# Performance work log

Hardware: AMD Instinct MI355X
Metric: run time of the kernel (lower is better)

Reference implementation:

```python
import jax, jax.numpy as jnp
import numpy as np
from jax import lax

ITER_ = 3
SMOOTH = 1e-05

B, C, D, H, W = 2, 3, 128, 160, 160


def _maxpool_axis(x, axis):
    # 3-wide max pool along one axis, stride 1, pad 1 (torch pads with -inf for max pool)
    win = [1] * x.ndim
    win[axis] = 3
    pad = [(0, 0)] * x.ndim
    pad[axis] = (1, 1)
    return lax.reduce_window(x, -jnp.inf, lax.max, tuple(win), (1,) * x.ndim, tuple(pad))


def _soft_erode(x):
    # min over axis-aligned erosions (erode = -maxpool(-x))
    nx = -x
    p1 = -_maxpool_axis(nx, 2)
    p2 = -_maxpool_axis(nx, 3)
    p3 = -_maxpool_axis(nx, 4)
    return jnp.minimum(jnp.minimum(p1, p2), p3)


def _soft_dilate(x):
    pad = ((0, 0), (0, 0), (1, 1), (1, 1), (1, 1))
    return lax.reduce_window(x, -jnp.inf, lax.max, (1, 1, 3, 3, 3), (1,) * 5, pad)


def _soft_open(x):
    return _soft_dilate(_soft_erode(x))


def _soft_skel(x):
    skel = jax.nn.relu(x - _soft_open(x))
    x_work = x
    for _ in range(ITER_):
        x_work = _soft_erode(x_work)
        delta = jax.nn.relu(x_work - _soft_open(x_work))
        skel = skel + jax.nn.relu(delta - skel * delta)
    return skel


def setup_inputs() -> dict:
    key = jax.random.key(0)
    k1, k2 = jax.random.split(key)
    net_output = jax.random.uniform(k1, (B, C, D, H, W), dtype=jnp.float32)
    target = jax.random.randint(k2, (B, 1, D, H, W), 0, C, dtype=jnp.int64)
    return {"net_output": net_output, "target": target}


def reference(net_output, target):
    num_classes = net_output.shape[1]
    labels = jnp.clip(target[:, 0], 0, num_classes - 1)
    target_1h = jax.nn.one_hot(labels, num_classes, dtype=net_output.dtype)  # [B,D,H,W,C]
    target_1h = jnp.moveaxis(target_1h, -1, 1)  # [B,C,D,H,W]

    # include_background=False, num_classes > 1 -> drop background channel
    pred = net_output[:, 1:]
    gt = target_1h[:, 1:]

    skel_pred = _soft_skel(pred)
    skel_gt = _soft_skel(gt)

    dims = (2, 3, 4)
    tprec = (jnp.sum(skel_pred * gt, dims) + SMOOTH) / (jnp.sum(skel_pred, dims) + SMOOTH)
    tsens = (jnp.sum(skel_gt * pred, dims) + SMOOTH) / (jnp.sum(skel_gt, dims) + SMOOTH)
    cl_dice = (2.0 * tprec * tsens + SMOOTH) / (tprec + tsens + SMOOTH)
    return 1.0 - jnp.mean(cl_dice)
```

## Files before the change

### kernel.cpp

```cpp
#include <hip/hip_runtime.h>
#include <math.h>

#define D_ 128
#define H_ 160
#define W_ 160
#define HW_ (H_ * W_)
#define V_ (D_ * H_ * W_)
#define SMOOTHF 1e-5

#define R_ 16
#define TY 10
#define ZC 16
#define COLS 40
#define NT 640
#define LROW 41
#define NYT 16
#define NZC 8
#define NTB (NYT * NZC)

__device__ __forceinline__ float max3f(float a, float b, float c) { return fmaxf(fmaxf(a, b), c); }
__device__ __forceinline__ float min3f(float a, float b, float c) { return fminf(fminf(a, b), c); }
__device__ __forceinline__ float4 f4min(float4 a, float4 b) {
    return make_float4(fminf(a.x,b.x), fminf(a.y,b.y), fminf(a.z,b.z), fminf(a.w,b.w));
}
__device__ __forceinline__ float4 f4max(float4 a, float4 b) {
    return make_float4(fmaxf(a.x,b.x), fmaxf(a.y,b.y), fmaxf(a.z,b.z), fmaxf(a.w,b.w));
}
__device__ __forceinline__ float4 min3x(float l, float4 c, float r) {
    return make_float4(min3f(l,c.x,c.y), min3f(c.x,c.y,c.z), min3f(c.y,c.z,c.w), min3f(c.z,c.w,r));
}
__device__ __forceinline__ float4 max3x(float l, float4 c, float r) {
    return make_float4(max3f(l,c.x,c.y), max3f(c.x,c.y,c.z), max3f(c.y,c.z,c.w), max3f(c.z,c.w,r));
}
__device__ __forceinline__ float4 relu4sub(float4 a, float4 b) {
    return make_float4(fmaxf(a.x-b.x,0.f), fmaxf(a.y-b.y,0.f), fmaxf(a.z-b.z,0.f), fmaxf(a.w-b.w,0.f));
}
__device__ __forceinline__ float4 skel_upd(float4 s, float4 d) {
    return make_float4(s.x + fmaxf(d.x - s.x*d.x, 0.f), s.y + fmaxf(d.y - s.y*d.y, 0.f),
                       s.z + fmaxf(d.z - s.z*d.z, 0.f), s.w + fmaxf(d.w - s.w*d.w, 0.f));
}

__device__ __forceinline__ float4 load_src4(const float* __restrict__ net,
                                            const int* __restrict__ tgt,
                                            int i, long p) {
    if (i < 4) {
        int b = i >> 1, c = (i & 1) + 1;
        return *(const float4*)(net + (long)(b * 3 + c) * V_ + p);
    } else {
        int j = i - 4;
        int b = j >> 1, c = (j & 1) + 1;
        int4 t = *(const int4*)(tgt + (long)b * V_ + p);
        float4 o;
        int tx = t.x < 0 ? 0 : (t.x > 2 ? 2 : t.x);
        int ty = t.y < 0 ? 0 : (t.y > 2 ? 2 : t.y);
        int tz = t.z < 0 ? 0 : (t.z > 2 ? 2 : t.z);
        int tw = t.w < 0 ? 0 : (t.w > 2 ? 2 : t.w);
        o.x = (tx == c) ? 1.0f : 0.0f;
        o.y = (ty == c) ? 1.0f : 0.0f;
        o.z = (tz == c) ? 1.0f : 0.0f;
        o.w = (tw == c) ? 1.0f : 0.0f;
        return o;
    }
}

template <int VAR>
__global__ __launch_bounds__(NT, 4) void fused_pair(
    const float* __restrict__ net, const int* __restrict__ tgt, int i0,
    const float* __restrict__ e_in, float* __restrict__ e_out,
    float* __restrict__ skel, float* __restrict__ partials) {

    __shared__ float4 Pb[2][R_ * LROW];
    __shared__ float4 E1b[2][R_ * LROW];
    __shared__ float4 E2b[R_ * LROW];
    __shared__ float smr[NT / 64][2];

    const int j = blockIdx.y, i = i0 + j;
    const int bx = blockIdx.x;
    const int y0 = (bx % NYT) * TY;
    const int z0 = (bx / NYT) * ZC;
    const int tid = threadIdx.x;
    const int r  = tid / COLS;
    const int x4 = tid - r * COLS;
    const int y  = y0 - 3 + r;
    const bool yok  = (y >= 0 && y < H_);
    const bool ymok = (y - 1 >= 0 && y - 1 < H_);
    const bool ypok = (y + 1 >= 0 && y + 1 < H_);
    const int rm = (r > 0) ? r - 1 : 0;
    const int rp = (r < R_ - 1) ? r + 1 : R_ - 1;
    const int xm = (x4 > 0) ? x4 - 1 : 0;
    const int xp = (x4 < COLS - 1) ? x4 + 1 : COLS - 1;
    const bool fxm = (x4 > 0), fxp = (x4 < COLS - 1);
    const bool rout = (r >= 3 && r < 3 + TY);
    const long colbase = (long)(yok ? y : 0) * W_ + x4 * 4;

    const float* ein_v = (VAR == 1) ? e_in + (long)j * V_ : nullptr;
    float* eout_v = (VAR == 0) ? e_out + (long)j * V_ : nullptr;
    float* skel_v = skel + (long)j * V_;
    const int ipart = (i < 4) ? (i + 4) : (i - 4);

    const float4 INF4  = make_float4( INFINITY,  INFINITY,  INFINITY,  INFINITY);
    const float4 NINF4 = make_float4(-INFINITY, -INFINITY, -INFINITY, -INFINITY);

    float4 a0 = INF4, a1 = INF4, a2 = INF4;
    float4 e11 = NINF4, e12 = NINF4;
    float4 x1a = NINF4, x1b = NINF4;
    float4 x2a = NINF4, x2b = NINF4;
    float4 psk = make_float4(0,0,0,0), ppr = make_float4(0,0,0,0);
    float acc0 = 0.f, acc1 = 0.f;

    for (int s = z0 - 3; s <= z0 + ZC + 2; ++s) {
        float4 anew;
        {
            const bool zok = (s >= 0 && s < D_);
            float4 v = INF4;
            if (zok && yok) {
                long p = (long)s * HW_ + colbase;
                v = (VAR == 0) ? load_src4(net, tgt, i, p)
                               : *(const float4*)(ein_v + p);
            }
            Pb[s & 1][r * LROW + x4] = v;
            anew = v;
            if (VAR == 1) {
                int z3 = s - 3;
                if (z3 >= z0 && z3 < z0 + ZC && rout) {
                    long p = (long)z3 * HW_ + colbase;
                    psk = *(const float4*)(skel_v + p);
                    ppr = load_src4(net, tgt, ipart, p);
                }
            }
        }

        float4 fe1;
        {
            const int z1 = s - 1;
            const bool z1ok = (z1 >= 0 && z1 < D_);
            const float4* Pp = Pb[z1 & 1];
            float4 up = Pp[rm * LROW + x4];
            float4 dn = Pp[rp * LROW + x4];
            float lf = Pp[r * LROW + xm].w;
            float rt = Pp[r * LROW + xp].x;
            if (!ymok) up = INF4;
            if (!ypok) dn = INF4;
            if (!fxm) lf = INFINITY;
            if (!fxp) rt = INFINITY;
            float4 e = f4min(f4min(min3x(lf, a2, rt), f4min(up, dn)), f4min(a1, anew));
            if (!z1ok || !yok) e = NINF4;
            fe1 = e;
            E1b[z1 & 1][r * LROW + x4] = e;
        }
        __syncthreads();

        float4 fe2, f1;
        {
            const int z2 = s - 2;
            const bool z2ok = (z2 >= 0 && z2 < D_);
            const float4* Ep = E1b[z2 & 1];
            float4 n00 = Ep[rm*LROW+xm], n01 = Ep[rm*LROW+x4], n02 = Ep[rm*LROW+xp];
            float4 n10 = Ep[r *LROW+xm],                        n12 = Ep[r *LROW+xp];
            float4 n20 = Ep[rp*LROW+xm], n21 = Ep[rp*LROW+x4], n22 = Ep[rp*LROW+xp];
            float4 c = e12;
            {
                float4 up = ymok ? n01 : INF4;
                float4 dn = ypok ? n21 : INF4;
                float lf = fxm ? n10.w : INFINITY;
                float rt = fxp ? n12.x : INFINITY;
                float4 zu = (z2 >= 1)     ? e11 : INF4;
                float4 zd = (z2 + 1 < D_) ? fe1 : INF4;
                float4 e = f4min(f4min(min3x(lf, c, rt), f4min(up, dn)), f4min(zu, zd));
                if (!z2ok || !yok) e = NINF4;
                fe2 = e;
            }
            {
                float l0 = fxm ? n00.w : -INFINITY, r0 = fxp ? n02.x : -INFINITY;
                float l1 = fxm ? n10.w : -INFINITY, r1 = fxp ? n12.x : -INFINITY;
                float l2 = fxm ? n20.w : -INFINITY, r2 = fxp ? n22.x : -INFINITY;
                float4 m = f4max(f4max(max3x(l0, n01, r0), max3x(l1, c, r1)), max3x(l2, n21, r2));
                if (!z2ok) m = NINF4;
                f1 = m;
            }
            E2b[r * LROW + x4] = fe2;
            if (VAR == 0 && z2 >= z0 && z2 < z0 + ZC && rout) {
                *(float4*)(eout_v + (long)z2 * HW_ + colbase) = fe2;
            }
        }
        __syncthreads();

        float4 f2;
        {
            float4 m00 = E2b[rm*LROW+xm], m01 = E2b[rm*LROW+x4], m02 = E2b[rm*LROW+xp];
            float4 m10 = E2b[r *LROW+xm],                         m12 = E2b[r *LROW+xp];
            float4 m20 = E2b[rp*LROW+xm], m21 = E2b[rp*LROW+x4], m22 = E2b[rp*LROW+xp];
            float l0 = fxm ? m00.w : -INFINITY, r0 = fxp ? m02.x : -INFINITY;
            float l1 = fxm ? m10.w : -INFINITY, r1 = fxp ? m12.x : -INFINITY;
            float l2 = fxm ? m20.w : -INFINITY, r2 = fxp ? m22.x : -INFINITY;
            f2 = f4max(f4max(max3x(l0, m01, r0), max3x(l1, fe2, r1)), max3x(l2, m21, r2));
        }
        {
            const int z3 = s - 3;
            if (z3 >= z0 && z3 < z0 + ZC && rout) {
                float4 dil1 = f4max(f4max(x1a, x1b), f1);
                float4 dil2 = f4max(f4max(x2a, x2b), f2);
                float4 cin = a0, ce1 = e11;
                long p = (long)z3 * HW_ + colbase;
                if (VAR == 0) {
                    float4 s0 = relu4sub(cin, dil1);
                    float4 d1 = relu4sub(ce1, dil2);
                    *(float4*)(skel_v + p) = skel_upd(s0, d1);
                } else {
                    float4 d2 = relu4sub(cin, dil1);
                    float4 sp = skel_upd(psk, d2);
                    float4 d3 = relu4sub(ce1, dil2);
                    float4 fin = skel_upd(sp, d3);
                    acc0 += fin.x * ppr.x + fin.y * ppr.y + fin.z * ppr.z + fin.w * ppr.w;
                    acc1 += fin.x + fin.y + fin.z + fin.w;
                }
            }
        }
        a0 = a1; a1 = a2; a2 = anew;
        e11 = e12; e12 = fe1;
        x1a = x1b; x1b = f1;
        x2a = x2b; x2b = f2;
    }

    if (VAR == 1) {
        #pragma unroll
        for (int off = 32; off > 0; off >>= 1) {
            acc0 += __shfl_down(acc0, off);
            acc1 += __shfl_down(acc1, off);
        }
        int wid = tid >> 6, lane = tid & 63;
        __syncthreads();
        if (lane == 0) { smr[wid][0] = acc0; smr[wid][1] = acc1; }
        __syncthreads();
        if (tid == 0) {
            float t0 = 0.f, t1 = 0.f;
            #pragma unroll
            for (int w = 0; w < NT / 64; ++w) { t0 += smr[w][0]; t1 += smr[w][1]; }
            long base = ((long)i * NTB + bx) * 2;
            partials[base + 0] = t0;
            partials[base + 1] = t1;
        }
    }
}

__global__ void reduce_partials_kernel(const float* __restrict__ partials,
                                       int i0,
                                       double* __restrict__ sums) {
    int i = i0 + blockIdx.x;
    int t = threadIdx.x;
    long base = ((long)i * NTB + t) * 2;
    double v0 = (double)partials[base + 0];
    double v1 = (double)partials[base + 1];
    #pragma unroll
    for (int off = 32; off > 0; off >>= 1) {
        v0 += __shfl_down(v0, off);
        v1 += __shfl_down(v1, off);
    }
    __shared__ double sm[2][2];
    int wid = t >> 6, lane = t & 63;
    if (lane == 0) { sm[wid][0] = v0; sm[wid][1] = v1; }
    __syncthreads();
    if (t == 0) {
        sums[2 * i + 0] = sm[0][0] + sm[1][0];
        sums[2 * i + 1] = sm[0][1] + sm[1][1];
    }
}

__global__ void finalize_kernel(const double* __restrict__ sums,
                                float* __restrict__ out) {
    if (threadIdx.x == 0 && blockIdx.x == 0) {
        double acc = 0.0;
        #pragma unroll
        for (int i = 0; i < 4; ++i) {
            double tprec = (sums[2 * i + 0] + SMOOTHF) / (sums[2 * i + 1] + SMOOTHF);
            double tsens = (sums[2 * (i + 4) + 0] + SMOOTHF) / (sums[2 * (i + 4) + 1] + SMOOTHF);
            double cl = (2.0 * tprec * tsens + SMOOTHF) / (tprec + tsens + SMOOTHF);
            acc += cl;
        }
        out[0] = (float)(1.0 - acc * 0.25);
    }
}

extern "C" void kernel_launch(void* const* d_in, const int* in_sizes, int n_in,
                              void* d_out, int out_size, void* d_ws, size_t ws_size,
                              hipStream_t stream) {
    const float* net = (const float*)d_in[0];
    const int* tgt = (const int*)d_in[1];
    float* out = (float*)d_out;

    char* ws = (char*)d_ws;
    double* sums = (double*)ws;
    float* partials = (float*)(ws + 256);
    size_t head = 256 + (size_t)8 * NTB * 2 * sizeof(float);
    head = (head + 255) & ~(size_t)255;
    float* base = (float*)(ws + head);

    size_t perVol = (size_t)2 * V_ * sizeof(float);
    int G = 1;
    if (ws_size >= head + perVol * 8) G = 8;
    else if (ws_size >= head + perVol * 4) G = 4;
    else if (ws_size >= head + perVol * 2) G = 2;

    dim3 blk(NT);
    dim3 grd(NTB, G);

    for (int i0 = 0; i0 < 8; i0 += G) {
        float* SKEL = base;
        float* E2buf = base + (size_t)G * V_;

        fused_pair<0><<<grd, blk, 0, stream>>>(net, tgt, i0, nullptr, E2buf, SKEL, nullptr);
        fused_pair<1><<<grd, blk, 0, stream>>>(net, tgt, i0, E2buf, nullptr, SKEL, partials);

        reduce_partials_kernel<<<G, 128, 0, stream>>>(partials, i0, sums);
    }

    finalize_kernel<<<1, 64, 0, stream>>>(sums, out);
}
```

Baseline: 342.3 us.

## Skew stencil pipeline stages to use one barrier per slab

Double-buffers the second erosion buffer and staggers the erode/dilate stages by one z-step so only a single __syncthreads per slab iteration is needed instead of two. The center input value and the skeleton/partner loads are now fetched from global memory at output time rather than carried in registers. This is meant to cut barrier stalls and register pressure. In exchange it adds an extra loop iteration, more shared memory, and redundant global reads.

```diff
diff --git a/kernel.cpp b/kernel.cpp
--- a/kernel.cpp
+++ b/kernel.cpp
@@ -71,7 +71,7 @@
 
     __shared__ float4 Pb[2][R_ * LROW];
     __shared__ float4 E1b[2][R_ * LROW];
-    __shared__ float4 E2b[R_ * LROW];
+    __shared__ float4 E2b[2][R_ * LROW];
     __shared__ float smr[NT / 64][2];
 
     const int j = blockIdx.y, i = i0 + j;
@@ -101,37 +101,27 @@
     const float4 INF4  = make_float4( INFINITY,  INFINITY,  INFINITY,  INFINITY);
     const float4 NINF4 = make_float4(-INFINITY, -INFINITY, -INFINITY, -INFINITY);
 
-    float4 a0 = INF4, a1 = INF4, a2 = INF4;
-    float4 e11 = NINF4, e12 = NINF4;
-    float4 x1a = NINF4, x1b = NINF4;
+    float4 p1 = INF4, p2 = INF4;
+    float4 b1 = NINF4, b2 = NINF4, b3 = NINF4;
+    float4 c1 = NINF4;
+    float4 x1a = NINF4, x1b = NINF4, x1c = NINF4;
     float4 x2a = NINF4, x2b = NINF4;
-    float4 psk = make_float4(0,0,0,0), ppr = make_float4(0,0,0,0);
     float acc0 = 0.f, acc1 = 0.f;
 
-    for (int s = z0 - 3; s <= z0 + ZC + 2; ++s) {
-        float4 anew;
-        {
+    for (int s = z0 - 3; s <= z0 + ZC + 3; ++s) {
+        float4 anew = INF4;
+        if (s <= z0 + ZC + 2) {
             const bool zok = (s >= 0 && s < D_);
-            float4 v = INF4;
             if (zok && yok) {
                 long p = (long)s * HW_ + colbase;
-                v = (VAR == 0) ? load_src4(net, tgt, i, p)
-                               : *(const float4*)(ein_v + p);
-            }
-            Pb[s & 1][r * LROW + x4] = v;
-            anew = v;
-            if (VAR == 1) {
-                int z3 = s - 3;
-                if (z3 >= z0 && z3 < z0 + ZC && rout) {
-                    long p = (long)z3 * HW_ + colbase;
-                    psk = *(const float4*)(skel_v + p);
-                    ppr = load_src4(net, tgt, ipart, p);
-                }
-            }
-        }
-
-        float4 fe1;
-        {
+                anew = (VAR == 0) ? load_src4(net, tgt, i, p)
+                                  : *(const float4*)(ein_v + p);
+            }
+            Pb[s & 1][r * LROW + x4] = anew;
+        }
+
+        float4 fe1 = NINF4;
+        if (s >= z0 - 1 && s <= z0 + ZC + 2) {
             const int z1 = s - 1;
             const bool z1ok = (z1 >= 0 && z1 < D_);
             const float4* Pp = Pb[z1 & 1];
@@ -143,70 +133,79 @@
             if (!ypok) dn = INF4;
             if (!fxm) lf = INFINITY;
             if (!fxp) rt = INFINITY;
-            float4 e = f4min(f4min(min3x(lf, a2, rt), f4min(up, dn)), f4min(a1, anew));
+            float4 e = f4min(f4min(min3x(lf, p1, rt), f4min(up, dn)), f4min(p2, anew));
             if (!z1ok || !yok) e = NINF4;
             fe1 = e;
             E1b[z1 & 1][r * LROW + x4] = e;
         }
-        __syncthreads();
-
-        float4 fe2, f1;
-        {
+
+        float4 fe2 = NINF4, f1 = NINF4;
+        if (s >= z0 + 1 && s <= z0 + ZC + 2) {
             const int z2 = s - 2;
             const bool z2ok = (z2 >= 0 && z2 < D_);
             const float4* Ep = E1b[z2 & 1];
-            float4 n00 = Ep[rm*LROW+xm], n01 = Ep[rm*LROW+x4], n02 = Ep[rm*LROW+xp];
-            float4 n10 = Ep[r *LROW+xm],                        n12 = Ep[r *LROW+xp];
-            float4 n20 = Ep[rp*LROW+xm], n21 = Ep[rp*LROW+x4], n22 = Ep[rp*LROW+xp];
-            float4 c = e12;
+            float4 n01 = Ep[rm * LROW + x4];
+            float4 n21 = Ep[rp * LROW + x4];
+            float4 c = b1;
+            float l0 = fxm ? Ep[rm * LROW + xm].w : -INFINITY;
+            float r0 = fxp ? Ep[rm * LROW + xp].x : -INFINITY;
+            float l1 = fxm ? Ep[r  * LROW + xm].w : -INFINITY;
+            float r1 = fxp ? Ep[r  * LROW + xp].x : -INFINITY;
+            float l2 = fxm ? Ep[rp * LROW + xm].w : -INFINITY;
+            float r2 = fxp ? Ep[rp * LROW + xp].x : -INFINITY;
             {
                 float4 up = ymok ? n01 : INF4;
                 float4 dn = ypok ? n21 : INF4;
-                float lf = fxm ? n10.w : INFINITY;
-                float rt = fxp ? n12.x : INFINITY;
-                float4 zu = (z2 >= 1)     ? e11 : INF4;
+                float lf = fxm ? l1 : INFINITY;
+                float rt = fxp ? r1 : INFINITY;
+                float4 zu = (z2 >= 1)     ? b2  : INF4;
                 float4 zd = (z2 + 1 < D_) ? fe1 : INF4;
                 float4 e = f4min(f4min(min3x(lf, c, rt), f4min(up, dn)), f4min(zu, zd));
                 if (!z2ok || !yok) e = NINF4;
                 fe2 = e;
             }
             {
-                float l0 = fxm ? n00.w : -INFINITY, r0 = fxp ? n02.x : -INFINITY;
-                float l1 = fxm ? n10.w : -INFINITY, r1 = fxp ? n12.x : -INFINITY;
-                float l2 = fxm ? n20.w : -INFINITY, r2 = fxp ? n22.x : -INFINITY;
                 float4 m = f4max(f4max(max3x(l0, n01, r0), max3x(l1, c, r1)), max3x(l2, n21, r2));
                 if (!z2ok) m = NINF4;
                 f1 = m;
             }
-            E2b[r * LROW + x4] = fe2;
+            E2b[z2 & 1][r * LROW + x4] = fe2;
             if (VAR == 0 && z2 >= z0 && z2 < z0 + ZC && rout) {
                 *(float4*)(eout_v + (long)z2 * HW_ + colbase) = fe2;
             }
         }
-        __syncthreads();
-
-        float4 f2;
+
+        float4 f2 = NINF4;
+        if (s >= z0 + 2) {
+            const int z3 = s - 3;
+            const float4* Eq = E2b[z3 & 1];
+            float4 m01 = Eq[rm * LROW + x4];
+            float4 m21 = Eq[rp * LROW + x4];
+            float l0 = fxm ? Eq[rm * LROW + xm].w : -INFINITY;
+            float r0 = fxp ? Eq[rm * LROW + xp].x : -INFINITY;
+            float l1 = fxm ? Eq[r  * LROW + xm].w : -INFINITY;
+            float r1 = fxp ? Eq[r  * LROW + xp].x : -INFINITY;
+            float l2 = fxm ? Eq[rp * LROW + xm].w : -INFINITY;
+            float r2 = fxp ? Eq[rp * LROW + xp].x : -INFINITY;
+            f2 = f4max(f4max(max3x(l0, m01, r0), max3x(l1, c1, r1)), max3x(l2, m21, r2));
+        }
+
         {
-            float4 m00 = E2b[rm*LROW+xm], m01 = E2b[rm*LROW+x4], m02 = E2b[rm*LROW+xp];
-            float4 m10 = E2b[r *LROW+xm],                         m12 = E2b[r *LROW+xp];
-            float4 m20 = E2b[rp*LROW+xm], m21 = E2b[rp*LROW+x4], m22 = E2b[rp*LROW+xp];
-            float l0 = fxm ? m00.w : -INFINITY, r0 = fxp ? m02.x : -INFINITY;
-            float l1 = fxm ? m10.w : -INFINITY, r1 = fxp ? m12.x : -INFINITY;
-            float l2 = fxm ? m20.w : -INFINITY, r2 = fxp ? m22.x : -INFINITY;
-            f2 = f4max(f4max(max3x(l0, m01, r0), max3x(l1, fe2, r1)), max3x(l2, m21, r2));
-        }
-        {
-            const int z3 = s - 3;
-            if (z3 >= z0 && z3 < z0 + ZC && rout) {
-                float4 dil1 = f4max(f4max(x1a, x1b), f1);
+            const int z = s - 4;
+            if (z >= z0 && z < z0 + ZC && rout) {
+                float4 dil1 = f4max(f4max(x1a, x1b), x1c);
                 float4 dil2 = f4max(f4max(x2a, x2b), f2);
-                float4 cin = a0, ce1 = e11;
-                long p = (long)z3 * HW_ + colbase;
+                float4 ce1 = b3;
+                long p = (long)z * HW_ + colbase;
                 if (VAR == 0) {
+                    float4 cin = load_src4(net, tgt, i, p);
                     float4 s0 = relu4sub(cin, dil1);
                     float4 d1 = relu4sub(ce1, dil2);
                     *(float4*)(skel_v + p) = skel_upd(s0, d1);
                 } else {
+                    float4 cin = *(const float4*)(ein_v + p);
+                    float4 psk = *(const float4*)(skel_v + p);
+                    float4 ppr = load_src4(net, tgt, ipart, p);
                     float4 d2 = relu4sub(cin, dil1);
                     float4 sp = skel_upd(psk, d2);
                     float4 d3 = relu4sub(ce1, dil2);
@@ -216,10 +215,14 @@
                 }
             }
         }
-        a0 = a1; a1 = a2; a2 = anew;
-        e11 = e12; e12 = fe1;
-        x1a = x1b; x1b = f1;
+
+        p2 = p1; p1 = anew;
+        b3 = b2; b2 = b1; b1 = fe1;
+        c1 = fe2;
+        x1a = x1b; x1b = x1c; x1c = f1;
         x2a = x2b; x2b = f2;
+
+        __syncthreads();
     }
 
     if (VAR == 1) {
```

Result: no change. 345.7 us (+1.0%).
